# Kernel tuning notes

Hardware: AMD Instinct MI355X
Metric: run time of the kernel (lower is better)

Reference implementation:

```python
import jax, jax.numpy as jnp
import numpy as np

B, T, I, H, O, L = 128, 1024, 256, 512, 256, 2


def setup_inputs() -> dict:
    key = jax.random.key(0)
    ks = jax.random.split(key, 12)
    s_in = 1.0 / np.sqrt(I)
    s_h = 1.0 / np.sqrt(H)
    return {
        "x": jax.random.normal(ks[0], (B, T, I), dtype=jnp.float32),
        "h0": jax.random.normal(ks[1], (B, H), dtype=jnp.float32),
        # layer 0: input_size -> hidden
        "W_ih0": jax.random.uniform(ks[2], (H, I), jnp.float32, -s_in, s_in),
        "b_ih0": jax.random.uniform(ks[3], (H,), jnp.float32, -s_in, s_in),
        "W_hh0": jax.random.uniform(ks[4], (H, H), jnp.float32, -s_h, s_h),
        "b_hh0": jax.random.uniform(ks[5], (H,), jnp.float32, -s_h, s_h),
        # layer 1: hidden -> hidden
        "W_ih1": jax.random.uniform(ks[6], (H, H), jnp.float32, -s_h, s_h),
        "b_ih1": jax.random.uniform(ks[7], (H,), jnp.float32, -s_h, s_h),
        "W_hh1": jax.random.uniform(ks[8], (H, H), jnp.float32, -s_h, s_h),
        "b_hh1": jax.random.uniform(ks[9], (H,), jnp.float32, -s_h, s_h),
        # output head
        "W_out": jax.random.uniform(ks[10], (O, H), jnp.float32, -s_h, s_h),
        "b_out": jax.random.uniform(ks[11], (O,), jnp.float32, -s_h, s_h),
    }


def reference(x, h0, W_ih0, b_ih0, W_hh0, b_hh0, W_ih1, b_ih1, W_hh1, b_hh1, W_out, b_out):
    """Returns Y: (B, T, O). Single hidden state h threaded through all layers,
    matching the original module's loop structure."""
    layers = ((W_ih0, b_ih0, W_hh0, b_hh0), (W_ih1, b_ih1, W_hh1, b_hh1))

    def step(h, x_t):  # h: (B,H), x_t: (B,I)
        inp = x_t
        for (Wih, bih, Whh, bhh) in layers:
            h = jnp.tanh(inp @ Wih.T + bih + h @ Whh.T + bhh)
            inp = h
        y = inp @ W_out.T + b_out  # (B, O)
        return h, y

    xs = jnp.swapaxes(x, 0, 1)  # (T, B, I)
    _, ys = jax.lax.scan(step, h0, xs)
    return jnp.swapaxes(ys, 0, 1)  # (B, T, O)
```

## Files before the change

### kernel.cpp

```cpp
#include <hip/hip_runtime.h>
#include <cstdint>
#include <cstddef>


typedef _Float16 f16;
typedef _Float16 f16x8 __attribute__((ext_vector_type(8)));
typedef float    f32x4 __attribute__((ext_vector_type(4)));

#define NB 128
#define NT 1024
#define NI 256
#define NH 512
#define NO 256

#define WS_WHH0 (size_t)(0)
#define WS_W1C  (size_t)(524288)
#define WS_WOUT (size_t)(1048576)
#define WS_WIH0 (size_t)(1310720)
#define WS_BC0  (size_t)(1572864)
#define WS_B1C  (size_t)(1574912)
#define WS_BOUT (size_t)(1576960)
#define WS_H1P  (size_t)(2097152)
#define WS_H2P  (size_t)(2621440)

#define AGENT __HIP_MEMORY_SCOPE_AGENT
#define SPIN_BUDGET (1 << 24)

__device__ __forceinline__ f32x4 mfma16(f16x8 a, f16x8 b, f32x4 c) {
  return __builtin_amdgcn_mfma_f32_16x16x32_f16(a, b, c, 0, 0, 0);
}

__device__ __forceinline__ float fast_tanh(float v) {
  float a = __builtin_fabsf(v);
  float e = __expf(-2.0f * a);
  float r = (1.0f - e) * __builtin_amdgcn_rcpf(1.0f + e);
  return v < 0.0f ? -r : r;
}

__device__ __forceinline__ uint32_t pack_h(float v, uint32_t tag) {
  union { f16 h; uint16_t u; } cv;
  cv.h = (f16)v;
  return ((uint32_t)cv.u << 16) | tag;
}

__device__ __forceinline__ void poll16(uint32_t* __restrict__ panel, int tid,
                                       uint32_t expect, uint32_t w[16],
                                       int* budget) {
  for (;;) {
    bool ok = true;
    #pragma unroll
    for (int i = 0; i < 16; i++) ok &= ((w[i] & 0xFFFFu) == expect);
    if (ok) return;
    if (--(*budget) < 0) return;
    __builtin_amdgcn_s_sleep(1);
    #pragma unroll
    for (int i = 0; i < 16; i++)
      w[i] = __hip_atomic_load(panel + tid + i * 512, __ATOMIC_RELAXED, AGENT);
  }
}

__global__ __launch_bounds__(256) void rnn9277_prep(
    const float* __restrict__ h0,
    const float* __restrict__ Wih0, const float* __restrict__ bih0,
    const float* __restrict__ Whh0, const float* __restrict__ bhh0,
    const float* __restrict__ Wih1, const float* __restrict__ bih1,
    const float* __restrict__ Whh1, const float* __restrict__ bhh1,
    const float* __restrict__ Woutp, const float* __restrict__ boutp,
    char* __restrict__ ws)
{
  const int tid = blockIdx.x * 256 + threadIdx.x;
  const int stride = gridDim.x * 256;
  f16* whh0 = (f16*)(ws + WS_WHH0);
  f16* w1c  = (f16*)(ws + WS_W1C);
  f16* wout = (f16*)(ws + WS_WOUT);
  f16* wih0 = (f16*)(ws + WS_WIH0);
  float* bc0 = (float*)(ws + WS_BC0);
  float* b1c = (float*)(ws + WS_B1C);
  float* bo  = (float*)(ws + WS_BOUT);
  uint32_t* h1p = (uint32_t*)(ws + WS_H1P);
  uint32_t* h2p = (uint32_t*)(ws + WS_H2P);

  for (int i = tid; i < NH * NH; i += stride) whh0[i] = (f16)Whh0[i];
  for (int i = tid; i < NH * NH; i += stride) w1c[i]  = (f16)(Wih1[i] + Whh1[i]);
  for (int i = tid; i < NO * NH; i += stride) wout[i] = (f16)Woutp[i];
  for (int i = tid; i < NH * NI; i += stride) wih0[i] = (f16)Wih0[i];
  for (int i = tid; i < NH; i += stride) { bc0[i] = bih0[i] + bhh0[i]; b1c[i] = bih1[i] + bhh1[i]; }
  for (int i = tid; i < NO; i += stride) bo[i] = boutp[i];

  for (int i = tid; i < 8 * 8192; i += stride)
    __hip_atomic_store(h1p + i, 0u, __ATOMIC_RELAXED, AGENT);
  for (int i = tid; i < NB * NH; i += stride) {
    int b = i >> 9, c = i & 511;
    int g = b >> 4, r = b & 15;
    union { f16 h; uint16_t u; } cv;
    cv.h = (f16)h0[i];
    __hip_atomic_store(h2p + (size_t)g * 8192 + r * 512 + c,
                       (uint32_t)cv.u << 16, __ATOMIC_RELAXED, AGENT);
  }
}

__global__ __launch_bounds__(512) void rnn9277_chain(
    const float* __restrict__ x, float* __restrict__ out, char* __restrict__ ws)
{
  const int wg = blockIdx.x;
  const bool isL0 = wg < 32;
  const int g = (wg & 31) >> 2, j = wg & 3;
  const int tid = threadIdx.x;
  const int wave = tid >> 6, lane = tid & 63;
  const int row16 = lane & 15, kq = lane >> 4;

  const f16* whh0 = (const f16*)(ws + WS_WHH0);
  const f16* w1c  = (const f16*)(ws + WS_W1C);
  const f16* wout = (const f16*)(ws + WS_WOUT);
  const f16* wih0 = (const f16*)(ws + WS_WIH0);
  const float* bc0 = (const float*)(ws + WS_BC0);
  const float* b1c = (const float*)(ws + WS_B1C);
  const float* bo  = (const float*)(ws + WS_BOUT);
  uint32_t* h1p = (uint32_t*)(ws + WS_H1P) + (size_t)g * 8192;
  uint32_t* h2p = (uint32_t*)(ws + WS_H2P) + (size_t)g * 8192;

  __shared__ __align__(16) f16 stage[2][16 * 520];

  int budget = SPIN_BUDGET;

  f16x8 Bh[16];
  f16x8 Bx[8];
  f16x8 By[16];
  float bias = 0.f, ybias = 0.f;
  {
    const int col = j * 128 + wave * 16 + row16;
    const f16* wp = (isL0 ? whh0 : w1c) + (size_t)col * NH + kq * 8;
    #pragma unroll
    for (int kk = 0; kk < 16; kk++) Bh[kk] = *(const f16x8*)(wp + kk * 32);
    bias = (isL0 ? bc0 : b1c)[col];
    if (isL0) {
      const f16* qp = wih0 + (size_t)col * NI + kq * 8;
      #pragma unroll
      for (int kk = 0; kk < 8; kk++) Bx[kk] = *(const f16x8*)(qp + kk * 32);
      if (wave < 4) {
        const int oc = j * 64 + wave * 16 + row16;
        const f16* rp = wout + (size_t)oc * NH + kq * 8;
        #pragma unroll
        for (int kk = 0; kk < 16; kk++) By[kk] = *(const f16x8*)(rp + kk * 32);
        ybias = bo[oc];
      }
    }
  }

  if (isL0) {
    for (int t = 0; t <= NT; ++t) {
      uint32_t w[16];
      #pragma unroll
      for (int i = 0; i < 16; i++)
        w[i] = __hip_atomic_load(h2p + tid + i * 512, __ATOMIC_RELAXED, AGENT);

      f32x4 accx = {0.f, 0.f, 0.f, 0.f};
      if (t < NT) {
        const float* xp = x + ((size_t)(g * 16 + row16) * NT + t) * NI + kq * 8;
        #pragma unroll
        for (int kk = 0; kk < 8; kk++) {
          f32x4 lo = *(const f32x4*)(xp + kk * 32);
          f32x4 hi = *(const f32x4*)(xp + kk * 32 + 4);
          f16x8 a;
          a[0] = (f16)lo[0]; a[1] = (f16)lo[1]; a[2] = (f16)lo[2]; a[3] = (f16)lo[3];
          a[4] = (f16)hi[0]; a[5] = (f16)hi[1]; a[6] = (f16)hi[2]; a[7] = (f16)hi[3];
          accx = mfma16(a, Bx[kk], accx);
        }
      }

      poll16(h2p, tid, (uint32_t)t, w, &budget);

      f16* st = &stage[t & 1][0];
      #pragma unroll
      for (int i = 0; i < 16; i++) {
        union { uint16_t u; f16 h; } cv;
        cv.u = (uint16_t)(w[i] >> 16);
        st[i * 520 + tid] = cv.h;
      }
      __syncthreads();

      const f16* ap = st + row16 * 520 + kq * 8;
      if (t < NT) {
        f32x4 acc2 = {0.f, 0.f, 0.f, 0.f};
        #pragma unroll
        for (int kk = 0; kk < 16; kk += 2) {
          accx = mfma16(*(const f16x8*)(ap + kk * 32), Bh[kk], accx);
          acc2 = mfma16(*(const f16x8*)(ap + (kk + 1) * 32), Bh[kk + 1], acc2);
        }
        const int col = j * 128 + wave * 16 + row16;
        const uint32_t tag = (uint32_t)(t + 1);
        #pragma unroll
        for (int rr = 0; rr < 4; rr++) {
          uint32_t wv = pack_h(fast_tanh(accx[rr] + acc2[rr] + bias), tag);
          __hip_atomic_store(h1p + (kq * 4 + rr) * 512 + col, wv,
                             __ATOMIC_RELAXED, AGENT);
        }
      }
      if (t > 0 && wave < 4) {
        f32x4 ya = {0.f, 0.f, 0.f, 0.f};
        #pragma unroll
        for (int kk = 0; kk < 16; kk++)
          ya = mfma16(*(const f16x8*)(ap + kk * 32), By[kk], ya);
        const int oc = j * 64 + wave * 16 + row16;
        #pragma unroll
        for (int rr = 0; rr < 4; rr++)
          out[((size_t)(g * 16 + kq * 4 + rr) * NT + (t - 1)) * NO + oc] = ya[rr] + ybias;
      }
    }
  } else {
    for (int t = 0; t < NT; ++t) {
      uint32_t w[16];
      #pragma unroll
      for (int i = 0; i < 16; i++)
        w[i] = __hip_atomic_load(h1p + tid + i * 512, __ATOMIC_RELAXED, AGENT);

      poll16(h1p, tid, (uint32_t)(t + 1), w, &budget);

      f16* st = &stage[t & 1][0];
      #pragma unroll
      for (int i = 0; i < 16; i++) {
        union { uint16_t u; f16 h; } cv;
        cv.u = (uint16_t)(w[i] >> 16);
        st[i * 520 + tid] = cv.h;
      }
      __syncthreads();

      const f16* ap = st + row16 * 520 + kq * 8;
      f32x4 a0 = {0.f, 0.f, 0.f, 0.f}, a1 = {0.f, 0.f, 0.f, 0.f};
      #pragma unroll
      for (int kk = 0; kk < 16; kk += 2) {
        a0 = mfma16(*(const f16x8*)(ap + kk * 32), Bh[kk], a0);
        a1 = mfma16(*(const f16x8*)(ap + (kk + 1) * 32), Bh[kk + 1], a1);
      }
      const int col = j * 128 + wave * 16 + row16;
      const uint32_t tag = (uint32_t)(t + 1);
      #pragma unroll
      for (int rr = 0; rr < 4; rr++) {
        uint32_t wv = pack_h(fast_tanh(a0[rr] + a1[rr] + bias), tag);
        __hip_atomic_store(h2p + (kq * 4 + rr) * 512 + col, wv,
                           __ATOMIC_RELAXED, AGENT);
      }
    }
  }
}

extern "C" void kernel_launch(void* const* d_in, const int* in_sizes, int n_in,
                              void* d_out, int out_size, void* d_ws, size_t ws_size,
                              hipStream_t stream) {
  const float* x    = (const float*)d_in[0];
  const float* h0   = (const float*)d_in[1];
  const float* Wih0 = (const float*)d_in[2];
  const float* bih0 = (const float*)d_in[3];
  const float* Whh0 = (const float*)d_in[4];
  const float* bhh0 = (const float*)d_in[5];
  const float* Wih1 = (const float*)d_in[6];
  const float* bih1 = (const float*)d_in[7];
  const float* Whh1 = (const float*)d_in[8];
  const float* bhh1 = (const float*)d_in[9];
  const float* Wout = (const float*)d_in[10];
  const float* bout = (const float*)d_in[11];
  char* ws = (char*)d_ws;
  float* out = (float*)d_out;

  rnn9277_prep<<<dim3(128), dim3(256), 0, stream>>>(
      h0, Wih0, bih0, Whh0, bhh0, Wih1, bih1, Whh1, bhh1, Wout, bout, ws);
  rnn9277_chain<<<dim3(64), dim3(512), 0, stream>>>(x, out, ws);
}
```

Before: 6.702 ms.

## Replace per-element tag polling with per-workgroup progress flags

Before fetching the hidden-state panel, one wave in each workgroup now spins on four per-workgroup progress counters instead of having every thread poll sixteen tagged words. After publishing its outputs, each producer workgroup hits a barrier and then bumps its flag. The fetch still checks tags and reloads only the stale elements, which covers the relaxed-ordering gap between the flag and the data. The change adds a barrier and a flag store per step, and shrinks the spin budget.

```diff
diff --git a/kernel.cpp b/kernel.cpp
--- a/kernel.cpp
+++ b/kernel.cpp
@@ -22,9 +22,10 @@
 #define WS_BOUT (size_t)(1576960)
 #define WS_H1P  (size_t)(2097152)
 #define WS_H2P  (size_t)(2621440)
+#define WS_FLG  (size_t)(3145728)
 
 #define AGENT __HIP_MEMORY_SCOPE_AGENT
-#define SPIN_BUDGET (1 << 24)
+#define SPIN_BUDGET (1 << 22)
 
 __device__ __forceinline__ f32x4 mfma16(f16x8 a, f16x8 b, f32x4 c) {
   return __builtin_amdgcn_mfma_f32_16x16x32_f16(a, b, c, 0, 0, 0);
@@ -43,19 +44,35 @@
   return ((uint32_t)cv.u << 16) | tag;
 }
 
-__device__ __forceinline__ void poll16(uint32_t* __restrict__ panel, int tid,
-                                       uint32_t expect, uint32_t w[16],
-                                       int* budget) {
+__device__ __forceinline__ void poll4(int* base, int target, int* budget) {
   for (;;) {
-    bool ok = true;
-    #pragma unroll
-    for (int i = 0; i < 16; i++) ok &= ((w[i] & 0xFFFFu) == expect);
-    if (ok) return;
+    int a = __hip_atomic_load(base,      __ATOMIC_RELAXED, AGENT);
+    int b = __hip_atomic_load(base + 16, __ATOMIC_RELAXED, AGENT);
+    int c = __hip_atomic_load(base + 32, __ATOMIC_RELAXED, AGENT);
+    int d = __hip_atomic_load(base + 48, __ATOMIC_RELAXED, AGENT);
+    if (a >= target && b >= target && c >= target && d >= target) return;
     if (--(*budget) < 0) return;
     __builtin_amdgcn_s_sleep(1);
+  }
+}
+
+__device__ __forceinline__ void fetch16(uint32_t* __restrict__ panel, int tid,
+                                        uint32_t expect, uint32_t w[16],
+                                        int* budget) {
+  #pragma unroll
+  for (int i = 0; i < 16; i++)
+    w[i] = __hip_atomic_load(panel + tid + i * 512, __ATOMIC_RELAXED, AGENT);
+  for (;;) {
+    int stale = 0;
     #pragma unroll
     for (int i = 0; i < 16; i++)
-      w[i] = __hip_atomic_load(panel + tid + i * 512, __ATOMIC_RELAXED, AGENT);
+      if ((w[i] & 0xFFFFu) != expect) stale |= (1 << i);
+    if (!stale) return;
+    if (--(*budget) < 0) return;
+    #pragma unroll
+    for (int i = 0; i < 16; i++)
+      if (stale & (1 << i))
+        w[i] = __hip_atomic_load(panel + tid + i * 512, __ATOMIC_RELAXED, AGENT);
   }
 }
 
@@ -79,6 +96,7 @@
   float* bo  = (float*)(ws + WS_BOUT);
   uint32_t* h1p = (uint32_t*)(ws + WS_H1P);
   uint32_t* h2p = (uint32_t*)(ws + WS_H2P);
+  int* flg = (int*)(ws + WS_FLG);
 
   for (int i = tid; i < NH * NH; i += stride) whh0[i] = (f16)Whh0[i];
   for (int i = tid; i < NH * NH; i += stride) w1c[i]  = (f16)(Wih1[i] + Whh1[i]);
@@ -86,6 +104,9 @@
   for (int i = tid; i < NH * NI; i += stride) wih0[i] = (f16)Wih0[i];
   for (int i = tid; i < NH; i += stride) { bc0[i] = bih0[i] + bhh0[i]; b1c[i] = bih1[i] + bhh1[i]; }
   for (int i = tid; i < NO; i += stride) bo[i] = boutp[i];
+
+  for (int i = tid; i < 1024; i += stride)
+    __hip_atomic_store(flg + i, 0, __ATOMIC_RELAXED, AGENT);
 
   for (int i = tid; i < 8 * 8192; i += stride)
     __hip_atomic_store(h1p + i, 0u, __ATOMIC_RELAXED, AGENT);
@@ -118,6 +139,8 @@
   const float* bo  = (const float*)(ws + WS_BOUT);
   uint32_t* h1p = (uint32_t*)(ws + WS_H1P) + (size_t)g * 8192;
   uint32_t* h2p = (uint32_t*)(ws + WS_H2P) + (size_t)g * 8192;
+  int* h1fb = (int*)(ws + WS_FLG) + g * 64;
+  int* h2fb = (int*)(ws + WS_FLG + 2048) + g * 64;
 
   __shared__ __align__(16) f16 stage[2][16 * 520];
 
@@ -149,11 +172,6 @@
 
   if (isL0) {
     for (int t = 0; t <= NT; ++t) {
-      uint32_t w[16];
-      #pragma unroll
-      for (int i = 0; i < 16; i++)
-        w[i] = __hip_atomic_load(h2p + tid + i * 512, __ATOMIC_RELAXED, AGENT);
-
       f32x4 accx = {0.f, 0.f, 0.f, 0.f};
       if (t < NT) {
         const float* xp = x + ((size_t)(g * 16 + row16) * NT + t) * NI + kq * 8;
@@ -167,9 +185,10 @@
           accx = mfma16(a, Bx[kk], accx);
         }
       }
-
-      poll16(h2p, tid, (uint32_t)t, w, &budget);
-
+      if (tid < 64) poll4(h2fb, t, &budget);
+      __syncthreads();
+      uint32_t w[16];
+      fetch16(h2p, tid, (uint32_t)t, w, &budget);
       f16* st = &stage[t & 1][0];
       #pragma unroll
       for (int i = 0; i < 16; i++) {
@@ -195,6 +214,10 @@
           __hip_atomic_store(h1p + (kq * 4 + rr) * 512 + col, wv,
                              __ATOMIC_RELAXED, AGENT);
         }
+        __builtin_amdgcn_s_barrier();
+        asm volatile("" ::: "memory");
+        if (tid == 0)
+          __hip_atomic_store(h1fb + j * 16, t + 1, __ATOMIC_RELAXED, AGENT);
       }
       if (t > 0 && wave < 4) {
         f32x4 ya = {0.f, 0.f, 0.f, 0.f};
@@ -209,13 +232,10 @@
     }
   } else {
     for (int t = 0; t < NT; ++t) {
+      if (tid < 64) poll4(h1fb, t + 1, &budget);
+      __syncthreads();
       uint32_t w[16];
-      #pragma unroll
-      for (int i = 0; i < 16; i++)
-        w[i] = __hip_atomic_load(h1p + tid + i * 512, __ATOMIC_RELAXED, AGENT);
-
-      poll16(h1p, tid, (uint32_t)(t + 1), w, &budget);
-
+      fetch16(h1p, tid, (uint32_t)(t + 1), w, &budget);
       f16* st = &stage[t & 1][0];
       #pragma unroll
       for (int i = 0; i < 16; i++) {
@@ -240,6 +260,10 @@
         __hip_atomic_store(h2p + (kq * 4 + rr) * 512 + col, wv,
                            __ATOMIC_RELAXED, AGENT);
       }
+      __builtin_amdgcn_s_barrier();
+      asm volatile("" ::: "memory");
+      if (tid == 0)
+        __hip_atomic_store(h2fb + j * 16, t + 1, __ATOMIC_RELAXED, AGENT);
     }
   }
 }
```

After: 7.363 ms. 9.9% more time.

## Replace spin polling with adaptive clock-paced waits and selective refetch

Applied to the files above, without the earlier changes.

The tag-polling loop between the layer-0 and layer-1 workgroups is replaced by two parts. Each wave first sleeps until an estimated ready time, read from s_memrealtime, with the period adapted up or down depending on whether the first check found stale data. It then refetches only the stale slots, without sleeping. This aims to cut memory-polling traffic and wasted sleep granularity on the critical inter-workgroup handoff. In exchange, a mis-estimated period can add latency. The smaller spin budget and the immediate refetch loop could also give up early and read stale values.

```diff
diff --git a/kernel.cpp b/kernel.cpp
--- a/kernel.cpp
+++ b/kernel.cpp
@@ -24,7 +24,7 @@
 #define WS_H2P  (size_t)(2621440)
 
 #define AGENT __HIP_MEMORY_SCOPE_AGENT
-#define SPIN_BUDGET (1 << 24)
+#define SPIN_BUDGET (1 << 22)
 
 __device__ __forceinline__ f32x4 mfma16(f16x8 a, f16x8 b, f32x4 c) {
   return __builtin_amdgcn_mfma_f32_16x16x32_f16(a, b, c, 0, 0, 0);
@@ -43,19 +43,32 @@
   return ((uint32_t)cv.u << 16) | tag;
 }
 
-__device__ __forceinline__ void poll16(uint32_t* __restrict__ panel, int tid,
-                                       uint32_t expect, uint32_t w[16],
-                                       int* budget) {
+__device__ __forceinline__ void wait_clock(uint64_t next_ready, int* budget) {
   for (;;) {
-    bool ok = true;
-    #pragma unroll
-    for (int i = 0; i < 16; i++) ok &= ((w[i] & 0xFFFFu) == expect);
-    if (ok) return;
+    uint64_t now = __builtin_amdgcn_s_memrealtime();
+    if ((int64_t)(now - next_ready) >= 0) return;
     if (--(*budget) < 0) return;
     __builtin_amdgcn_s_sleep(1);
+  }
+}
+
+__device__ __forceinline__ void check_refetch16(uint32_t* __restrict__ panel,
+                                                int tid, uint32_t expect,
+                                                uint32_t w[16], int* budget,
+                                                int* stale_first) {
+  int first = 1;
+  for (;;) {
+    int stale = 0;
     #pragma unroll
     for (int i = 0; i < 16; i++)
-      w[i] = __hip_atomic_load(panel + tid + i * 512, __ATOMIC_RELAXED, AGENT);
+      if ((w[i] & 0xFFFFu) != expect) stale |= (1 << i);
+    if (first) { *stale_first = (stale != 0); first = 0; }
+    if (!stale) return;
+    if (--(*budget) < 0) return;
+    #pragma unroll
+    for (int i = 0; i < 16; i++)
+      if (stale & (1 << i))
+        w[i] = __hip_atomic_load(panel + tid + i * 512, __ATOMIC_RELAXED, AGENT);
   }
 }
 
@@ -123,6 +136,10 @@
 
   int budget = SPIN_BUDGET;
 
+  uint64_t next_ready = 0;
+  int period = 120;
+  const int P_MAX = 1500, P_UP = 16, P_DN = 2;
+
   f16x8 Bh[16];
   f16x8 Bx[8];
   f16x8 By[16];
@@ -149,6 +166,7 @@
 
   if (isL0) {
     for (int t = 0; t <= NT; ++t) {
+      wait_clock(next_ready, &budget);
       uint32_t w[16];
       #pragma unroll
       for (int i = 0; i < 16; i++)
@@ -168,18 +186,26 @@
         }
       }
 
-      poll16(h2p, tid, (uint32_t)t, w, &budget);
-
-      f16* st = &stage[t & 1][0];
+      int stale_first = 0;
+      check_refetch16(h2p, tid, (uint32_t)t, w, &budget, &stale_first);
+      {
+        uint64_t done = __builtin_amdgcn_s_memrealtime();
+        int st = __any(stale_first) ? 1 : 0;
+        period = st ? (period + P_UP > P_MAX ? P_MAX : period + P_UP)
+                    : (period - P_DN < 0 ? 0 : period - P_DN);
+        next_ready = done + (uint64_t)period;
+      }
+
+      f16* st16 = &stage[t & 1][0];
       #pragma unroll
       for (int i = 0; i < 16; i++) {
         union { uint16_t u; f16 h; } cv;
         cv.u = (uint16_t)(w[i] >> 16);
-        st[i * 520 + tid] = cv.h;
+        st16[i * 520 + tid] = cv.h;
       }
       __syncthreads();
 
-      const f16* ap = st + row16 * 520 + kq * 8;
+      const f16* ap = st16 + row16 * 520 + kq * 8;
       if (t < NT) {
         f32x4 acc2 = {0.f, 0.f, 0.f, 0.f};
         #pragma unroll
@@ -209,23 +235,32 @@
     }
   } else {
     for (int t = 0; t < NT; ++t) {
+      wait_clock(next_ready, &budget);
       uint32_t w[16];
       #pragma unroll
       for (int i = 0; i < 16; i++)
         w[i] = __hip_atomic_load(h1p + tid + i * 512, __ATOMIC_RELAXED, AGENT);
 
-      poll16(h1p, tid, (uint32_t)(t + 1), w, &budget);
-
-      f16* st = &stage[t & 1][0];
+      int stale_first = 0;
+      check_refetch16(h1p, tid, (uint32_t)(t + 1), w, &budget, &stale_first);
+      {
+        uint64_t done = __builtin_amdgcn_s_memrealtime();
+        int st = __any(stale_first) ? 1 : 0;
+        period = st ? (period + P_UP > P_MAX ? P_MAX : period + P_UP)
+                    : (period - P_DN < 0 ? 0 : period - P_DN);
+        next_ready = done + (uint64_t)period;
+      }
+
+      f16* st16 = &stage[t & 1][0];
       #pragma unroll
       for (int i = 0; i < 16; i++) {
         union { uint16_t u; f16 h; } cv;
         cv.u = (uint16_t)(w[i] >> 16);
-        st[i * 520 + tid] = cv.h;
+        st16[i * 520 + tid] = cv.h;
       }
       __syncthreads();
 
-      const f16* ap = st + row16 * 520 + kq * 8;
+      const f16* ap = st16 + row16 * 520 + kq * 8;
       f32x4 a0 = {0.f, 0.f, 0.f, 0.f}, a1 = {0.f, 0.f, 0.f, 0.f};
       #pragma unroll
       for (int kk = 0; kk < 16; kk += 2) {
```

After: 9.490 ms. +41.6%, slower.
